# Optimization experiments

Hardware: AMD Instinct MI355X
Metric: run time of the kernel (lower is better)

The kernel has to match this reference:

```python
import jax, jax.numpy as jnp
import numpy as np

B, S, D = 8, 1024, 256
H, DH = 8, 32  # num_heads, head_dim; H*DH == D


def setup_inputs() -> dict:
    key = jax.random.key(0)
    ks = jax.random.split(key, 10)
    s = 0.02
    return {
        "q": jax.random.normal(ks[0], (B, S, D), jnp.float32),
        "k": jax.random.normal(ks[1], (B, S, D), jnp.float32),
        "v": jax.random.normal(ks[2], (B, S, D), jnp.float32),
        "mask": jnp.zeros((B, 1, 1, S), jnp.float32),  # additive mask
        "bias": jax.random.normal(ks[3], (1, H, S, S), jnp.float32),  # pair bias
        "Wq": jax.random.normal(ks[4], (H * DH, D), jnp.float32) * s,
        "Wk": jax.random.normal(ks[5], (H * DH, D), jnp.float32) * s,
        "Wv": jax.random.normal(ks[6], (H * DH, D), jnp.float32) * s,
        "Wg": jnp.zeros((H * DH, D), jnp.float32),   # gating init: zeros weight
        "bg": jnp.ones((H * DH,), jnp.float32),      # gating init: ones bias
        "Wo": jax.random.normal(ks[7], (D, H * DH), jnp.float32) * s,
    }


def reference(q, k, v, mask, bias, Wq, Wk, Wv, Wg, bg, Wo):
    norm = DH ** -0.5
    g = jnp.einsum('bsd,ed->bse', q, Wg) + bg            # [B,S,H*DH]
    qh = (jnp.einsum('bsd,ed->bse', q, Wq) * norm).reshape(B, S, H, DH)
    kh = jnp.einsum('bsd,ed->bse', k, Wk).reshape(B, S, H, DH)
    vh = jnp.einsum('bsd,ed->bse', v, Wv).reshape(B, S, H, DH)
    # scores [B,H,Q,K] with additive mask and pair bias (unicore softmax_dropout)
    attn = jnp.einsum('bqhd,bkhd->bhqk', qh, kh) + mask + bias
    attn = jax.nn.softmax(attn, axis=-1)
    o = jnp.einsum('bhqk,bkhd->bqhd', attn, vh).reshape(B, S, H * DH)
    o = jax.nn.sigmoid(g) * o                            # gating
    return jnp.einsum('bse,de->bsd', o, Wo)              # output proj, NO bias in fwd
```

## Files before the change

### kernel.cpp

```cpp
#include <hip/hip_runtime.h>


typedef __attribute__((ext_vector_type(4))) float f32x4;
typedef __attribute__((ext_vector_type(8))) unsigned short u16x8;
typedef __attribute__((ext_vector_type(4))) unsigned short u16x4;
typedef __attribute__((ext_vector_type(8))) __bf16 bf16x8;
typedef __attribute__((ext_vector_type(4))) __bf16 bf16x4;

#define BB 8
#define SS 1024
#define DD 256
#define HH 8
#define DHD 32

__device__ __forceinline__ float b2f(unsigned short s) {
  unsigned u = ((unsigned)s) << 16;
  return __builtin_bit_cast(float, u);
}
__device__ __forceinline__ f32x4 mfma16(u16x8 a, u16x8 b, f32x4 c) {
  return __builtin_amdgcn_mfma_f32_16x16x32_bf16(
      __builtin_bit_cast(bf16x8, a), __builtin_bit_cast(bf16x8, b), c, 0, 0, 0);
}

__device__ __forceinline__ void gload_lds16(const unsigned short* gsrc,
                                            unsigned short* ldst) {
#if __has_builtin(__builtin_amdgcn_global_load_lds)
  __builtin_amdgcn_global_load_lds(
      (const __attribute__((address_space(1))) unsigned int*)gsrc,
      (__attribute__((address_space(3))) unsigned int*)ldst, 16, 0, 0);
#else
  *(u16x8*)ldst = *(const u16x8*)gsrc;
#endif
}

__global__ __launch_bounds__(256) void proj_kernel(
    const float* __restrict__ q, const float* __restrict__ k,
    const float* __restrict__ v,
    const float* __restrict__ Wq, const float* __restrict__ Wg,
    const float* __restrict__ Wk, const float* __restrict__ Wv,
    const float* __restrict__ bg,
    unsigned short* __restrict__ qh, unsigned short* __restrict__ kh,
    unsigned short* __restrict__ vhT, unsigned short* __restrict__ sig) {
  const int slot = blockIdx.z;
  const float* A = (slot <= 1) ? q : (slot == 2 ? k : v);
  const float* W = (slot == 0) ? Wq : (slot == 1 ? Wg : (slot == 2 ? Wk : Wv));
  const int row0 = blockIdx.x * 64, col0 = blockIdx.y * 64;
  const int tid = threadIdx.x;
  const int w = tid >> 6, lane = tid & 63, g = lane >> 4, c = lane & 15;
  const int sr = tid >> 2, sc = tid & 3;

  __shared__ alignas(16) unsigned short As[64 * 32];
  __shared__ alignas(16) unsigned short Ws[64 * 32];

  const f32x4 zero = {0.f, 0.f, 0.f, 0.f};
  f32x4 acc[4] = {zero, zero, zero, zero};

  for (int kk = 0; kk < 8; ++kk) {
    __syncthreads();
    {
      const float* ap = A + (size_t)(row0 + sr) * DD + kk * 32 + sc * 8;
      f32x4 f0 = *(const f32x4*)ap;
      f32x4 f1 = *(const f32x4*)(ap + 4);
      bf16x8 a8;
#pragma unroll
      for (int j = 0; j < 4; ++j) { a8[j] = (__bf16)f0[j]; a8[j + 4] = (__bf16)f1[j]; }
      ((u16x8*)As)[sr * 4 + (sc ^ ((sr >> 1) & 3))] = __builtin_bit_cast(u16x8, a8);

      const float* wp = W + (size_t)(col0 + sr) * DD + kk * 32 + sc * 8;
      f32x4 w0 = *(const f32x4*)wp;
      f32x4 w1 = *(const f32x4*)(wp + 4);
      bf16x8 w8;
#pragma unroll
      for (int j = 0; j < 4; ++j) { w8[j] = (__bf16)w0[j]; w8[j + 4] = (__bf16)w1[j]; }
      ((u16x8*)Ws)[sr * 4 + (sc ^ ((sr >> 1) & 3))] = __builtin_bit_cast(u16x8, w8);
    }
    __syncthreads();
    const int arow = 16 * w + c;
    u16x8 af = ((u16x8*)As)[arow * 4 + (g ^ ((arow >> 1) & 3))];
#pragma unroll
    for (int n = 0; n < 4; ++n) {
      const int brow = 16 * n + c;
      u16x8 wf = ((u16x8*)Ws)[brow * 4 + (g ^ ((brow >> 1) & 3))];
      acc[n] = mfma16(af, wf, acc[n]);
    }
  }

  if (slot == 3) {
    const int row_base = row0 + 16 * w + 4 * g;
    const int bb = row_base >> 10;
    const int s0 = row_base & 1023;
#pragma unroll
    for (int n = 0; n < 4; ++n) {
      const int col = col0 + 16 * n + c;
      bf16x4 pv;
#pragma unroll
      for (int r = 0; r < 4; ++r) pv[r] = (__bf16)acc[n][r];
      *(u16x4*)(vhT + (size_t)(bb * 256 + col) * SS + s0) =
          __builtin_bit_cast(u16x4, pv);
    }
  } else {
#pragma unroll
    for (int n = 0; n < 4; ++n) {
#pragma unroll
      for (int r = 0; r < 4; ++r) {
        const int row = row0 + 16 * w + 4 * g + r;
        const int col = col0 + 16 * n + c;
        const size_t idx = (size_t)row * DD + col;
        const float val = acc[n][r];
        if (slot == 0)
          qh[idx] = __builtin_bit_cast(unsigned short,
                        (__bf16)(val * 0.17677669529663687f));
        else if (slot == 1)
          sig[idx] = __builtin_bit_cast(unsigned short,
                         (__bf16)(1.0f / (1.0f + __expf(-(val + bg[col])))));
        else
          kh[idx] = __builtin_bit_cast(unsigned short, (__bf16)val);
      }
    }
  }
}

__global__ __launch_bounds__(256, 4) void attn_kernel(
    const unsigned short* __restrict__ qh, const unsigned short* __restrict__ kh,
    const unsigned short* __restrict__ vhT, const unsigned short* __restrict__ sig,
    const float* __restrict__ mask, const float* __restrict__ bias,
    unsigned short* __restrict__ og) {
  const int bid = blockIdx.x;
  const int widx = (bid & 7) * 128 + (bid >> 3);
  const int h = widx >> 7, b = (widx >> 4) & 7, qt = widx & 15;
  const int tid = threadIdx.x;
  const int w = tid >> 6, lane = tid & 63, g = lane >> 4, c = lane & 15;

  __shared__ alignas(16) unsigned short KsB[2][64 * 32];
  __shared__ alignas(16) unsigned short VtB[2][32 * 64];
  __shared__ alignas(16) unsigned short Ps[4][16 * 64];
  unsigned short* P = Ps[w];

  const int q0 = qt * 64 + w * 16;
  const u16x8 qf =
      *(const u16x8*)(qh + (size_t)(b * SS + q0 + c) * DD + h * DHD + g * 8);

  const f32x4 zero = {0.f, 0.f, 0.f, 0.f};
  f32x4 acc[2] = {zero, zero};
  float m_r = -1e30f, l_r = 0.f;

  const float* maskb = mask + b * SS;
  const float* biasb = bias + (size_t)(h * SS + q0 + c) * SS;

  const unsigned short* kg = kh + (size_t)(b * SS + (tid >> 2)) * DD +
                             h * DHD + ((tid & 3) ^ ((tid >> 3) & 3)) * 8;
  const unsigned short* vg =
      vhT + (size_t)((b * HH + h) * DHD + (tid >> 3)) * SS +
      ((tid & 7) ^ ((tid >> 3) & 7)) * 8;

  gload_lds16(kg, KsB[0] + tid * 8);
  gload_lds16(vg, VtB[0] + tid * 8);
  f32x4 bi_c[4], mk_c[4];
#pragma unroll
  for (int t = 0; t < 4; ++t) {
    bi_c[t] = *(const f32x4*)(biasb + 16 * t + 4 * g);
    mk_c[t] = *(const f32x4*)(maskb + 16 * t + 4 * g);
  }
  __syncthreads();

  for (int kt = 0; kt < 16; ++kt) {
    const int cur = kt & 1;
    const int kv0 = kt * 64;
    f32x4 bi_n[4], mk_n[4];
    if (kt < 15) {
      gload_lds16(kg + (size_t)(kv0 + 64) * DD, KsB[cur ^ 1] + tid * 8);
      gload_lds16(vg + kv0 + 64, VtB[cur ^ 1] + tid * 8);
#pragma unroll
      for (int t = 0; t < 4; ++t) {
        bi_n[t] = *(const f32x4*)(biasb + kv0 + 64 + 16 * t + 4 * g);
        mk_n[t] = *(const f32x4*)(maskb + kv0 + 64 + 16 * t + 4 * g);
      }
    }

    const u16x8* Ks16 = (const u16x8*)KsB[cur];
    const u16x8* Vt16 = (const u16x8*)VtB[cur];

    f32x4 sv[4];
#pragma unroll
    for (int t = 0; t < 4; ++t) {
      const u16x8 kf = Ks16[(16 * t + c) * 4 + (g ^ ((c >> 1) & 3))];
      sv[t] = mfma16(kf, qf, zero);
    }
#pragma unroll
    for (int t = 0; t < 4; ++t) {
      sv[t] += mk_c[t];
      sv[t] += bi_c[t];
    }
    float pm = fmaxf(fmaxf(sv[0][0], sv[0][1]), fmaxf(sv[0][2], sv[0][3]));
#pragma unroll
    for (int t = 1; t < 4; ++t)
      pm = fmaxf(pm, fmaxf(fmaxf(sv[t][0], sv[t][1]), fmaxf(sv[t][2], sv[t][3])));
    if (!__all(pm - m_r <= 8.0f)) {
      float mx = fmaxf(pm, __shfl_xor(pm, 16));
      mx = fmaxf(mx, __shfl_xor(mx, 32));
      const float mnew = fmaxf(m_r, mx);
      const float scale = __expf(m_r - mnew);
      l_r *= scale;
      acc[0] *= scale;
      acc[1] *= scale;
      m_r = mnew;
    }
    float ps = 0.f;
#pragma unroll
    for (int t = 0; t < 4; ++t)
#pragma unroll
      for (int r = 0; r < 4; ++r) {
        const float p = __expf(sv[t][r] - m_r);
        sv[t][r] = p;
        ps += p;
      }
    l_r += ps;
#pragma unroll
    for (int t = 0; t < 4; ++t) {
      bf16x4 pv;
#pragma unroll
      for (int r = 0; r < 4; ++r) pv[r] = (__bf16)sv[t][r];
      const int n = 2 * t + (g >> 1);
      *(u16x4*)(P + c * 64 + ((n ^ (c & 7)) << 3) + ((g & 1) << 2)) =
          __builtin_bit_cast(u16x4, pv);
    }
#pragma unroll
    for (int s2 = 0; s2 < 2; ++s2) {
      const u16x8 pf =
          *(const u16x8*)(P + c * 64 + (((4 * s2 + g) ^ (c & 7)) << 3));
#pragma unroll
      for (int dt = 0; dt < 2; ++dt) {
        const u16x8 vf = Vt16[(16 * dt + c) * 8 + ((s2 * 4 + g) ^ (c & 7))];
        acc[dt] = mfma16(vf, pf, acc[dt]);
      }
    }
    if (kt < 15) {
      __syncthreads();
#pragma unroll
      for (int t = 0; t < 4; ++t) { bi_c[t] = bi_n[t]; mk_c[t] = mk_n[t]; }
    }
  }

  float l = l_r + __shfl_xor(l_r, 16);
  l += __shfl_xor(l, 32);
  const float inv = 1.0f / l;
#pragma unroll
  for (int dt = 0; dt < 2; ++dt) {
    const size_t idx =
        (size_t)(b * SS + q0 + c) * DD + h * DHD + 16 * dt + 4 * g;
    const u16x4 sg = *(const u16x4*)(sig + idx);
    bf16x4 ov;
#pragma unroll
    for (int r = 0; r < 4; ++r) ov[r] = (__bf16)(acc[dt][r] * inv * b2f(sg[r]));
    *(u16x4*)(og + idx) = __builtin_bit_cast(u16x4, ov);
  }
}

__global__ __launch_bounds__(256) void outproj_kernel(
    const unsigned short* __restrict__ og, const float* __restrict__ Wo,
    float* __restrict__ out) {
  const int row0 = blockIdx.x * 64, col0 = blockIdx.y * 64;
  const int tid = threadIdx.x;
  const int w = tid >> 6, lane = tid & 63, g = lane >> 4, c = lane & 15;
  const int sr = tid >> 2, sc = tid & 3;

  __shared__ alignas(16) unsigned short As[64 * 32];
  __shared__ alignas(16) unsigned short Ws[64 * 32];

  const f32x4 zero = {0.f, 0.f, 0.f, 0.f};
  f32x4 acc[4] = {zero, zero, zero, zero};

  for (int kk = 0; kk < 8; ++kk) {
    __syncthreads();
    {
      const unsigned short* ap = og + (size_t)(row0 + sr) * DD + kk * 32 + sc * 8;
      ((u16x8*)As)[sr * 4 + (sc ^ ((sr >> 1) & 3))] = *(const u16x8*)ap;

      const float* wp = Wo + (size_t)(col0 + sr) * DD + kk * 32 + sc * 8;
      f32x4 w0 = *(const f32x4*)wp;
      f32x4 w1 = *(const f32x4*)(wp + 4);
      bf16x8 w8;
#pragma unroll
      for (int j = 0; j < 4; ++j) { w8[j] = (__bf16)w0[j]; w8[j + 4] = (__bf16)w1[j]; }
      ((u16x8*)Ws)[sr * 4 + (sc ^ ((sr >> 1) & 3))] = __builtin_bit_cast(u16x8, w8);
    }
    __syncthreads();
    const int arow = 16 * w + c;
    u16x8 af = ((u16x8*)As)[arow * 4 + (g ^ ((arow >> 1) & 3))];
#pragma unroll
    for (int n = 0; n < 4; ++n) {
      const int brow = 16 * n + c;
      u16x8 wf = ((u16x8*)Ws)[brow * 4 + (g ^ ((brow >> 1) & 3))];
      acc[n] = mfma16(af, wf, acc[n]);
    }
  }

#pragma unroll
  for (int n = 0; n < 4; ++n) {
#pragma unroll
    for (int r = 0; r < 4; ++r) {
      const int row = row0 + 16 * w + 4 * g + r;
      const int col = col0 + 16 * n + c;
      out[(size_t)row * DD + col] = acc[n][r];
    }
  }
}

extern "C" void kernel_launch(void* const* d_in, const int* in_sizes, int n_in,
                              void* d_out, int out_size, void* d_ws,
                              size_t ws_size, hipStream_t stream) {
  const float* q    = (const float*)d_in[0];
  const float* k    = (const float*)d_in[1];
  const float* v    = (const float*)d_in[2];
  const float* mask = (const float*)d_in[3];
  const float* bias = (const float*)d_in[4];
  const float* Wq   = (const float*)d_in[5];
  const float* Wk   = (const float*)d_in[6];
  const float* Wv   = (const float*)d_in[7];
  const float* Wg   = (const float*)d_in[8];
  const float* bg   = (const float*)d_in[9];
  const float* Wo   = (const float*)d_in[10];
  float* out = (float*)d_out;

  char* ws = (char*)d_ws;
  unsigned short* qh  = (unsigned short*)(ws);
  unsigned short* kh  = (unsigned short*)(ws + (4u << 20));
  unsigned short* vhT = (unsigned short*)(ws + (8u << 20));
  unsigned short* sig = (unsigned short*)(ws + (12u << 20));
  unsigned short* og  = (unsigned short*)(ws + (16u << 20));

  hipLaunchKernelGGL(proj_kernel, dim3(128, 4, 4), dim3(256), 0, stream,
                     q, k, v, Wq, Wg, Wk, Wv, bg, qh, kh, vhT, sig);
  hipLaunchKernelGGL(attn_kernel, dim3(1024), dim3(256), 0, stream,
                     qh, kh, vhT, sig, mask, bias, og);
  hipLaunchKernelGGL(outproj_kernel, dim3(128, 4), dim3(256), 0, stream,
                     og, Wo, out);
}
```

Baseline: 80.39 us.

## Enlarge attention KV tile to 256 and cut block syncs per sweep

The attention kernel now stages 256 keys/values per double-buffered LDS tile instead of 64, so it runs four outer iterations with an inner unrolled loop over 64-key groups. This cuts the number of __syncthreads and prefetch phases. Bias and mask are now loaded directly inside the inner loop instead of being prefetched one tile ahead. The larger LDS footprint (about 72KB) lowers the occupancy target to 2 blocks per CU and may expose the latency of the bias loads.

```diff
diff --git a/kernel.cpp b/kernel.cpp
--- a/kernel.cpp
+++ b/kernel.cpp
@@ -120,7 +120,7 @@
   }
 }
 
-__global__ __launch_bounds__(256, 4) void attn_kernel(
+__global__ __launch_bounds__(256, 2) void attn_kernel(
     const unsigned short* __restrict__ qh, const unsigned short* __restrict__ kh,
     const unsigned short* __restrict__ vhT, const unsigned short* __restrict__ sig,
     const float* __restrict__ mask, const float* __restrict__ bias,
@@ -131,8 +131,8 @@
   const int tid = threadIdx.x;
   const int w = tid >> 6, lane = tid & 63, g = lane >> 4, c = lane & 15;
 
-  __shared__ alignas(16) unsigned short KsB[2][64 * 32];
-  __shared__ alignas(16) unsigned short VtB[2][32 * 64];
+  __shared__ alignas(16) unsigned short KsB[2][256 * 32];
+  __shared__ alignas(16) unsigned short VtB[2][32 * 256];
   __shared__ alignas(16) unsigned short Ps[4][16 * 64];
   unsigned short* P = Ps[w];
 
@@ -147,98 +147,98 @@
   const float* maskb = mask + b * SS;
   const float* biasb = bias + (size_t)(h * SS + q0 + c) * SS;
 
-  const unsigned short* kg = kh + (size_t)(b * SS + (tid >> 2)) * DD +
-                             h * DHD + ((tid & 3) ^ ((tid >> 3) & 3)) * 8;
-  const unsigned short* vg =
-      vhT + (size_t)((b * HH + h) * DHD + (tid >> 3)) * SS +
-      ((tid & 7) ^ ((tid >> 3) & 7)) * 8;
-
-  gload_lds16(kg, KsB[0] + tid * 8);
-  gload_lds16(vg, VtB[0] + tid * 8);
-  f32x4 bi_c[4], mk_c[4];
-#pragma unroll
-  for (int t = 0; t < 4; ++t) {
-    bi_c[t] = *(const f32x4*)(biasb + 16 * t + 4 * g);
-    mk_c[t] = *(const f32x4*)(maskb + 16 * t + 4 * g);
-  }
+  auto stage = [&](int buf, int kv0) {
+    unsigned short* Kb = KsB[buf];
+    unsigned short* Vb = VtB[buf];
+#pragma unroll
+    for (int i = 0; i < 4; ++i) {
+      const int s = i * 256 + tid;
+      const int krow = s >> 2, kc = s & 3;
+      const int klc = kc ^ ((krow >> 1) & 3);
+      gload_lds16(kh + (size_t)(b * SS + kv0 + krow) * DD + h * DHD + klc * 8,
+                  Kb + s * 8);
+      const int vr = s >> 5, jp = s & 31;
+      const int jl = (jp & 24) | ((jp & 7) ^ (vr & 7));
+      gload_lds16(vhT + (size_t)((b * HH + h) * DHD + vr) * SS + kv0 + jl * 8,
+                  Vb + s * 8);
+    }
+  };
+
+  stage(0, 0);
   __syncthreads();
 
-  for (int kt = 0; kt < 16; ++kt) {
+#pragma unroll 1
+  for (int kt = 0; kt < 4; ++kt) {
     const int cur = kt & 1;
-    const int kv0 = kt * 64;
-    f32x4 bi_n[4], mk_n[4];
-    if (kt < 15) {
-      gload_lds16(kg + (size_t)(kv0 + 64) * DD, KsB[cur ^ 1] + tid * 8);
-      gload_lds16(vg + kv0 + 64, VtB[cur ^ 1] + tid * 8);
-#pragma unroll
-      for (int t = 0; t < 4; ++t) {
-        bi_n[t] = *(const f32x4*)(biasb + kv0 + 64 + 16 * t + 4 * g);
-        mk_n[t] = *(const f32x4*)(maskb + kv0 + 64 + 16 * t + 4 * g);
-      }
-    }
+    const int kv0 = kt * 256;
+    if (kt < 3) stage(cur ^ 1, kv0 + 256);
 
     const u16x8* Ks16 = (const u16x8*)KsB[cur];
     const u16x8* Vt16 = (const u16x8*)VtB[cur];
 
-    f32x4 sv[4];
-#pragma unroll
-    for (int t = 0; t < 4; ++t) {
-      const u16x8 kf = Ks16[(16 * t + c) * 4 + (g ^ ((c >> 1) & 3))];
-      sv[t] = mfma16(kf, qf, zero);
-    }
-#pragma unroll
-    for (int t = 0; t < 4; ++t) {
-      sv[t] += mk_c[t];
-      sv[t] += bi_c[t];
-    }
-    float pm = fmaxf(fmaxf(sv[0][0], sv[0][1]), fmaxf(sv[0][2], sv[0][3]));
-#pragma unroll
-    for (int t = 1; t < 4; ++t)
-      pm = fmaxf(pm, fmaxf(fmaxf(sv[t][0], sv[t][1]), fmaxf(sv[t][2], sv[t][3])));
-    if (!__all(pm - m_r <= 8.0f)) {
-      float mx = fmaxf(pm, __shfl_xor(pm, 16));
-      mx = fmaxf(mx, __shfl_xor(mx, 32));
-      const float mnew = fmaxf(m_r, mx);
-      const float scale = __expf(m_r - mnew);
-      l_r *= scale;
-      acc[0] *= scale;
-      acc[1] *= scale;
-      m_r = mnew;
-    }
-    float ps = 0.f;
-#pragma unroll
-    for (int t = 0; t < 4; ++t)
-#pragma unroll
-      for (int r = 0; r < 4; ++r) {
-        const float p = __expf(sv[t][r] - m_r);
-        sv[t][r] = p;
-        ps += p;
-      }
-    l_r += ps;
-#pragma unroll
-    for (int t = 0; t < 4; ++t) {
-      bf16x4 pv;
-#pragma unroll
-      for (int r = 0; r < 4; ++r) pv[r] = (__bf16)sv[t][r];
-      const int n = 2 * t + (g >> 1);
-      *(u16x4*)(P + c * 64 + ((n ^ (c & 7)) << 3) + ((g & 1) << 2)) =
-          __builtin_bit_cast(u16x4, pv);
-    }
-#pragma unroll
-    for (int s2 = 0; s2 < 2; ++s2) {
-      const u16x8 pf =
-          *(const u16x8*)(P + c * 64 + (((4 * s2 + g) ^ (c & 7)) << 3));
-#pragma unroll
-      for (int dt = 0; dt < 2; ++dt) {
-        const u16x8 vf = Vt16[(16 * dt + c) * 8 + ((s2 * 4 + g) ^ (c & 7))];
-        acc[dt] = mfma16(vf, pf, acc[dt]);
-      }
-    }
-    if (kt < 15) {
-      __syncthreads();
-#pragma unroll
-      for (int t = 0; t < 4; ++t) { bi_c[t] = bi_n[t]; mk_c[t] = mk_n[t]; }
-    }
+#pragma unroll
+    for (int gr = 0; gr < 4; ++gr) {
+      const int kvg = kv0 + gr * 64;
+      f32x4 sv[4];
+#pragma unroll
+      for (int t = 0; t < 4; ++t) {
+        const u16x8 kf =
+            Ks16[(gr * 64 + 16 * t + c) * 4 + (g ^ ((c >> 1) & 3))];
+        sv[t] = mfma16(kf, qf, zero);
+      }
+#pragma unroll
+      for (int t = 0; t < 4; ++t) {
+        const f32x4 bi = *(const f32x4*)(biasb + kvg + 16 * t + 4 * g);
+        const f32x4 mk = *(const f32x4*)(maskb + kvg + 16 * t + 4 * g);
+        sv[t] += bi + mk;
+      }
+      float pm = fmaxf(fmaxf(sv[0][0], sv[0][1]), fmaxf(sv[0][2], sv[0][3]));
+#pragma unroll
+      for (int t = 1; t < 4; ++t)
+        pm = fmaxf(pm,
+                   fmaxf(fmaxf(sv[t][0], sv[t][1]), fmaxf(sv[t][2], sv[t][3])));
+      if (!__all(pm - m_r <= 8.0f)) {
+        float mx = fmaxf(pm, __shfl_xor(pm, 16));
+        mx = fmaxf(mx, __shfl_xor(mx, 32));
+        const float mnew = fmaxf(m_r, mx);
+        const float scale = __expf(m_r - mnew);
+        l_r *= scale;
+        acc[0] *= scale;
+        acc[1] *= scale;
+        m_r = mnew;
+      }
+      float ps = 0.f;
+#pragma unroll
+      for (int t = 0; t < 4; ++t)
+#pragma unroll
+        for (int r = 0; r < 4; ++r) {
+          const float p = __expf(sv[t][r] - m_r);
+          sv[t][r] = p;
+          ps += p;
+        }
+      l_r += ps;
+#pragma unroll
+      for (int t = 0; t < 4; ++t) {
+        bf16x4 pv;
+#pragma unroll
+        for (int r = 0; r < 4; ++r) pv[r] = (__bf16)sv[t][r];
+        const int n = 2 * t + (g >> 1);
+        *(u16x4*)(P + c * 64 + ((n ^ (c & 7)) << 3) + ((g & 1) << 2)) =
+            __builtin_bit_cast(u16x4, pv);
+      }
+#pragma unroll
+      for (int s2 = 0; s2 < 2; ++s2) {
+        const u16x8 pf =
+            *(const u16x8*)(P + c * 64 + (((4 * s2 + g) ^ (c & 7)) << 3));
+#pragma unroll
+        for (int dt = 0; dt < 2; ++dt) {
+          const u16x8 vf =
+              Vt16[(16 * dt + c) * 32 + gr * 8 + ((4 * s2 + g) ^ (c & 7))];
+          acc[dt] = mfma16(vf, pf, acc[dt]);
+        }
+      }
+    }
+    __syncthreads();
   }
 
   float l = l_r + __shfl_xor(l_r, 16);
```

Result: no change. 80.24 us (-0.2%).
